# Kernel optimization log

Measured on AMD Instinct MI355X. Metric: run time of the kernel, lower is better.

## Reference

```python
import jax, jax.numpy as jnp
import numpy as np

jax.config.update("jax_enable_x64", True)  # window_sum runs cumsums in double, as in the torch source

WIN = 7
EPS = 0.01


def _gradient(I):
    # forward finite differences, cropping to [D-1, H-1, W-1] (same=False path, reduction='mean')
    c = I[:, :, 1:, 1:, 1:]
    dx = c - I[:, :, :-1, 1:, 1:]
    dy = c - I[:, :, 1:, :-1, 1:]
    dz = c - I[:, :, 1:, 1:, :-1]
    return dx, dy, dz


def _window_sum(I, win):
    # 3D box-filter via triple cumsum on a zero-padded double-precision volume
    if win == 1:
        return I
    half = win // 2
    pad = (half + win % 2, half)
    Ip = jnp.pad(I, ((0, 0), (0, 0), pad, pad, pad)).astype(jnp.float64)
    cs = jnp.cumsum(jnp.cumsum(jnp.cumsum(Ip, axis=2), axis=3), axis=4)
    x, y, z = I.shape[2:]
    w = win
    out = (cs[:, :, w:, w:, w:] - cs[:, :, w:, w:, :z] - cs[:, :, w:, :y, w:]
           - cs[:, :, :x, w:, w:] + cs[:, :, w:, :y, :z] + cs[:, :, :x, w:, :z]
           + cs[:, :, :x, :y, w:] - cs[:, :, :x, :y, :z])
    return out.astype(jnp.float32)


def setup_inputs() -> dict:
    key = jax.random.key(0)
    k1, k2 = jax.random.split(key)
    shape = (2, 1, 160, 192, 160)
    Ii = jax.random.normal(k1, shape, dtype=jnp.float32)
    Ji = jax.random.normal(k2, shape, dtype=jnp.float32)
    return {"Ii": Ii, "Ji": Ji}


def reference(Ii, Ji):
    def det(dx, dy, dz):
        return dx * dx + dy * dy + dz * dz + EPS

    dxI, dyI, dzI = _gradient(Ii)
    dxJ, dyJ, dzJ = _gradient(Ji)
    dx_I = _window_sum(dxI, WIN)
    dy_I = _window_sum(dyI, WIN)
    dz_I = _window_sum(dzI, WIN)
    dx_J = _window_sum(dxJ, WIN)
    dy_J = _window_sum(dyJ, WIN)
    dz_J = _window_sum(dzJ, WIN)
    cross = jnp.abs(dx_I * dx_J + dy_I * dy_J + dz_I * dz_J) + EPS
    norm = jnp.sqrt(det(dx_I, dy_I, dz_I) * det(dx_J, dy_J, dz_J))
    return jnp.mean(cross / norm)
```

## Files before the change

kernel.cpp:

```cpp
#include <hip/hip_runtime.h>

#define IYD 192
#define IZD 160
#define PLANE 30720
#define VOLSZ 4915200
#define YG 191
#define ZG 159

#define RAW_V 660
#define RAW_R 44
#define ZB 1320
#define DB 2400
#define ZD_V 540
#define ZD_R 36
#define TB 3480
#define WB 3992
#define LDSF 4504

#define NVOX_INV (1.0f / 9657342.0f)

__global__ __launch_bounds__(256, 4) void grad_sim_tele(
    const float* __restrict__ Ii, const float* __restrict__ Ji,
    float* __restrict__ out)
{
    __shared__ __align__(16) float lds[LDSF];
    const int tid = threadIdx.x;
    const int z0 = (int)blockIdx.x * 32;
    const int y0 = (int)blockIdx.y * 8;
    const int seg = blockIdx.z & 7;
    const int bat = blockIdx.z >> 3;
    const int s0 = seg * 20;
    const int a0 = (seg == 0) ? 0 : (s0 - 3);
    const int aLast = (seg == 7) ? 159 : (s0 + 23);

    const float* __restrict__ bI = Ii + (size_t)bat * VOLSZ;
    const float* __restrict__ bJ = Ji + (size_t)bat * VOLSZ;

    const float* gp[5];
    int lof[5];
    bool okl[5];
#pragma unroll
    for (int k = 0; k < 5; ++k) {
        int idx = tid + 256 * k;
        bool inr = idx < 1170;
        int id2 = inr ? idx : 0;
        int v = id2 / 585;
        int r = id2 - v * 585;
        int yy = r / 39;
        int zz = r - yy * 39;
        int iy = y0 - 3 + yy;
        int iz = z0 - 3 + zz;
        okl[k] = inr && ((unsigned)iy < IYD) && ((unsigned)iz < IZD);
        int iyc = min(max(iy, 0), IYD - 1);
        int izc = min(max(iz, 0), IZD - 1);
        gp[k] = (v ? bJ : bI) + (iyc * IZD + izc);
        lof[k] = inr ? (v * RAW_V + yy * RAW_R + zz) : 43;
    }

    const int zv = tid / 60;
    const int zrr = tid - 60 * zv;
    const int zr = zrr >> 2;
    const int zq = zrr & 3;
    const bool doZ = tid < 120;
    const bool zlo = (z0 == 0) && (zq == 0);
    const bool zhi = (z0 == 128) && (zq == 3);
    const int rawRd = zv * RAW_V + zr * RAW_R + 8 * zq;
    const int zdWr = zv * ZD_V + zr * ZD_R + 8 * zq;

    const bool doY = tid < 128;
    const int yf = tid >> 5;
    const int yv = yf & 1;
    const int yisW = yf >> 1;
    const int ybase = (yisW ? DB : ZB) + yv * ZD_V + (tid & 31);
    const int yout = (yisW ? WB : TB) + yv * 256 + (tid & 31);

    const int oy = tid >> 5;
    const int oz = tid & 31;
    const int ygl = y0 + oy;
    const int vmax = min(3, 190 - ygl);
    const int vmin = max(-3, -ygl);
    const int relHi = oy + vmax + 4;
    const int relLo = oy + vmin + 3;
    const int vHiI = ZB + relHi * ZD_R + oz;
    const int vLoI = ZB + relLo * ZD_R + oz;
    const bool okyz = (ygl < YG) && ((z0 + oz) < ZG);

    float Tr[2][8], Vr[2][8], Wr[2][8], Sdy[2], Sdz[2];
#pragma unroll
    for (int v = 0; v < 2; ++v) {
#pragma unroll
        for (int j = 0; j < 8; ++j) { Tr[v][j] = 0.f; Vr[v][j] = 0.f; Wr[v][j] = 0.f; }
        Sdy[v] = 0.f; Sdz[v] = 0.f;
    }
    float acc = 0.f;

    {
        const int pb = a0 * PLANE;
        float t[5];
#pragma unroll
        for (int k = 0; k < 5; ++k) t[k] = gp[k][pb];
#pragma unroll
        for (int k = 0; k < 5; ++k) lds[lof[k]] = okl[k] ? t[k] : 0.f;
    }
    __syncthreads();

    for (int ag = (a0 & ~7); ag <= aLast; ag += 8) {
#pragma unroll
        for (int p = 0; p < 8; ++p) {
            const int a = ag + p;
            if (a < a0 || a > aLast) continue;

            const bool dof = (a + 1) <= aLast;
            float pf[5];
            if (dof) {
                const int pb = (a + 1) * PLANE;
#pragma unroll
                for (int k = 0; k < 5; ++k) pf[k] = gp[k][pb];
            }
            if (doZ) {
                float C[16];
                const float4* rb = (const float4*)&lds[rawRd];
#pragma unroll
                for (int u = 0; u < 4; ++u) ((float4*)C)[u] = rb[u];
                float D[8];
#pragma unroll
                for (int i = 0; i < 8; ++i) D[i] = C[i + 7] - C[i];
                if (zlo) { D[0] = C[7] - C[3]; D[1] = C[8] - C[3]; D[2] = C[9] - C[3]; }
                if (zhi) { D[4] = C[10] - C[4]; D[5] = C[10] - C[5];
                           D[6] = C[10] - C[6]; D[7] = C[10] - C[7]; }
                if (zlo) { C[1] = 0.f; C[2] = 0.f; C[3] = 0.f; }
                if (zhi) { C[11] = 0.f; C[12] = 0.f; C[13] = 0.f; C[14] = 0.f; }
                float Z[8];
                float w = C[1] + C[2] + C[3] + C[4] + C[5] + C[6] + C[7];
                Z[0] = w;
#pragma unroll
                for (int m = 1; m < 8; ++m) { w += C[m + 7] - C[m]; Z[m] = w; }
                float4* zb = (float4*)&lds[ZB + zdWr];
                zb[0] = make_float4(Z[0], Z[1], Z[2], Z[3]);
                zb[1] = make_float4(Z[4], Z[5], Z[6], Z[7]);
                float4* db = (float4*)&lds[DB + zdWr];
                db[0] = make_float4(D[0], D[1], D[2], D[3]);
                db[1] = make_float4(D[4], D[5], D[6], D[7]);
            }
            __syncthreads();

            if (doY) {
                float h[15];
#pragma unroll
                for (int r = 1; r < 15; ++r) h[r] = lds[ybase + r * ZD_R];
                if (y0 == 0)   { h[1] = 0.f; h[2] = 0.f; h[3] = 0.f; }
                if (y0 == 184) { h[11] = 0.f; h[12] = 0.f; h[13] = 0.f; h[14] = 0.f; }
                float w = h[1] + h[2] + h[3] + h[4] + h[5] + h[6] + h[7];
                lds[yout] = w;
#pragma unroll
                for (int q = 1; q < 8; ++q) {
                    w += h[q + 7] - h[q];
                    lds[yout + q * 32] = w;
                }
            }
            __syncthreads();

            {
                float tI = lds[TB + tid];
                float tJ = lds[TB + 256 + tid];
                float wI = lds[WB + tid];
                float wJ = lds[WB + 256 + tid];
                float vI = lds[vHiI] - lds[vLoI];
                float vJ = lds[vHiI + ZD_V] - lds[vLoI + ZD_V];
                if (a == a0) { vI = 0.f; vJ = 0.f; wI = 0.f; wJ = 0.f; }
                const int p1 = (p + 1) & 7;
                float hdxI = tI - Tr[0][p1];
                float hdxJ = tJ - Tr[1][p1];
                Sdy[0] += vI - Vr[0][p1]; Vr[0][p] = vI;
                Sdy[1] += vJ - Vr[1][p1]; Vr[1][p] = vJ;
                Sdz[0] += wI - Wr[0][p1]; Wr[0][p] = wI;
                Sdz[1] += wJ - Wr[1][p1]; Wr[1][p] = wJ;
                Tr[0][p] = tI; Tr[1][p] = tJ;
                if (p == 0) {
                    if (a == 0) {
                        Tr[0][5] = tI; Tr[0][6] = tI; Tr[0][7] = tI;
                        Tr[1][5] = tJ; Tr[1][6] = tJ; Tr[1][7] = tJ;
                    }
                }
                if (a >= s0 + 4) {
                    float cross = fabsf(hdxI * hdxJ + Sdy[0] * Sdy[1] + Sdz[0] * Sdz[1]) + 0.01f;
                    float dI = hdxI * hdxI + Sdy[0] * Sdy[0] + Sdz[0] * Sdz[0] + 0.01f;
                    float dJ = hdxJ * hdxJ + Sdy[1] * Sdy[1] + Sdz[1] * Sdz[1] + 0.01f;
                    float val = cross * rsqrtf(dI * dJ);
                    if (okyz) acc += val;
                }
            }
            if (dof) {
#pragma unroll
                for (int k = 0; k < 5; ++k) lds[lof[k]] = okl[k] ? pf[k] : 0.f;
            }
            __syncthreads();
        }
    }

    if (seg == 7) {
#pragma unroll
        for (int t = 0; t < 3; ++t) {
            const int sl = t + 1;
            float hdxI = Tr[0][7] - Tr[0][sl];
            float hdxJ = Tr[1][7] - Tr[1][sl];
            Sdy[0] -= Vr[0][sl]; Sdy[1] -= Vr[1][sl];
            Sdz[0] -= Wr[0][sl]; Sdz[1] -= Wr[1][sl];
            float cross = fabsf(hdxI * hdxJ + Sdy[0] * Sdy[1] + Sdz[0] * Sdz[1]) + 0.01f;
            float dI = hdxI * hdxI + Sdy[0] * Sdy[0] + Sdz[0] * Sdz[0] + 0.01f;
            float dJ = hdxJ * hdxJ + Sdy[1] * Sdy[1] + Sdz[1] * Sdz[1] + 0.01f;
            float val = cross * rsqrtf(dI * dJ);
            if (okyz) acc += val;
        }
    }

#pragma unroll
    for (int off = 32; off > 0; off >>= 1) acc += __shfl_down(acc, off, 64);
    __syncthreads();
    if ((tid & 63) == 0) lds[tid >> 6] = acc;
    __syncthreads();
    if (tid == 0)
        atomicAdd(out, (lds[0] + lds[1] + lds[2] + lds[3]) * NVOX_INV);
}

extern "C" void kernel_launch(void* const* d_in, const int* in_sizes, int n_in,
                              void* d_out, int out_size, void* d_ws, size_t ws_size,
                              hipStream_t stream) {
    const float* Ii = (const float*)d_in[0];
    const float* Ji = (const float*)d_in[1];
    float* out = (float*)d_out;
    hipMemsetAsync(d_out, 0, sizeof(float) * (out_size > 0 ? out_size : 1), stream);
    dim3 grid(5, 24, 16);
    grad_sim_tele<<<grid, dim3(256), 0, stream>>>(Ii, Ji, out);
}
```

Baseline: 86.21 us.

## Restructure box-filter pipeline with 64-wide z tiles and direct float4 global loads

```diff
diff --git a/kernel.cpp b/kernel.cpp
--- a/kernel.cpp
+++ b/kernel.cpp
@@ -7,82 +7,118 @@
 #define YG 191
 #define ZG 159
 
-#define RAW_V 660
-#define RAW_R 44
-#define ZB 1320
-#define DB 2400
-#define ZD_V 540
-#define ZD_R 36
-#define TB 3480
-#define WB 3992
-#define LDSF 4504
+#define ZBV 1020
+#define ZBR 68
+#define YBB 2040
+#define YBV 608
+#define YBR 76
+#define TBB 3256
+#define TBV 544
+#define TBR 68
+#define LDSF 4344
 
 #define NVOX_INV (1.0f / 9657342.0f)
 
-__global__ __launch_bounds__(256, 4) void grad_sim_tele(
+__device__ __forceinline__ float4 f4add(float4 a, float4 b) {
+    return make_float4(a.x + b.x, a.y + b.y, a.z + b.z, a.w + b.w);
+}
+__device__ __forceinline__ float4 f4sub(float4 a, float4 b) {
+    return make_float4(a.x - b.x, a.y - b.y, a.z - b.z, a.w - b.w);
+}
+__device__ __forceinline__ float4 f4scale(float4 a, float s) {
+    return make_float4(a.x * s, a.y * s, a.z * s, a.w * s);
+}
+
+__global__ __launch_bounds__(512, 4) void grad_sim_v9(
     const float* __restrict__ Ii, const float* __restrict__ Ji,
     float* __restrict__ out)
 {
     __shared__ __align__(16) float lds[LDSF];
     const int tid = threadIdx.x;
-    const int z0 = (int)blockIdx.x * 32;
-    const int y0 = (int)blockIdx.y * 8;
-    const int seg = blockIdx.z & 7;
-    const int bat = blockIdx.z >> 3;
-    const int s0 = seg * 20;
+    const int y0 = (int)blockIdx.x * 8;
+    const int z0 = (int)blockIdx.y * 64;
+    const int seg = blockIdx.z % 6;
+    const int bat = blockIdx.z / 6;
+    const int s0 = seg * 27;
     const int a0 = (seg == 0) ? 0 : (s0 - 3);
-    const int aLast = (seg == 7) ? 159 : (s0 + 23);
+    const int aLast = (seg == 5) ? 159 : (s0 + 30);
 
     const float* __restrict__ bI = Ii + (size_t)bat * VOLSZ;
     const float* __restrict__ bJ = Ji + (size_t)bat * VOLSZ;
 
-    const float* gp[5];
-    int lof[5];
-    bool okl[5];
-#pragma unroll
-    for (int k = 0; k < 5; ++k) {
-        int idx = tid + 256 * k;
-        bool inr = idx < 1170;
-        int id2 = inr ? idx : 0;
-        int v = id2 / 585;
-        int r = id2 - v * 585;
-        int yy = r / 39;
-        int zz = r - yy * 39;
-        int iy = y0 - 3 + yy;
-        int iz = z0 - 3 + zz;
-        okl[k] = inr && ((unsigned)iy < IYD) && ((unsigned)iz < IZD);
-        int iyc = min(max(iy, 0), IYD - 1);
-        int izc = min(max(iz, 0), IZD - 1);
-        gp[k] = (v ? bJ : bI) + (iyc * IZD + izc);
-        lof[k] = inr ? (v * RAW_V + yy * RAW_R + zz) : 43;
-    }
-
-    const int zv = tid / 60;
-    const int zrr = tid - 60 * zv;
-    const int zr = zrr >> 2;
-    const int zq = zrr & 3;
-    const bool doZ = tid < 120;
-    const bool zlo = (z0 == 0) && (zq == 0);
-    const bool zhi = (z0 == 128) && (zq == 3);
-    const int rawRd = zv * RAW_V + zr * RAW_R + 8 * zq;
-    const int zdWr = zv * ZD_V + zr * ZD_R + 8 * zq;
-
-    const bool doY = tid < 128;
-    const int yf = tid >> 5;
-    const int yv = yf & 1;
-    const int yisW = yf >> 1;
-    const int ybase = (yisW ? DB : ZB) + yv * ZD_V + (tid & 31);
-    const int yout = (yisW ? WB : TB) + yv * 256 + (tid & 31);
-
-    const int oy = tid >> 5;
-    const int oz = tid & 31;
+    const bool doZB = tid < 240;
+    {
+    }
+    const int e1t = doZB ? tid : 0;
+    const int e1v = e1t / 120;
+    const int e1r = (e1t % 120) >> 3;
+    const int e1o = e1t & 7;
+    const int e1iy = y0 - 3 + e1r;
+    const float e1my = (e1iy >= 0 && e1iy <= 191) ? 1.f : 0.f;
+    const int e1yc = min(max(e1iy, 0), 191);
+    const float* e1p0; const float* e1p1; const float* e1p2; const float* e1p3;
+    float e1m0, e1m1, e1m2, e1m3;
+    {
+        const float* vb = (e1v ? bJ : bI) + e1yc * IZD;
+        int zb;
+        zb = z0 + 8 * e1o - 4;
+        e1m0 = ((zb >= 0) && (zb + 3 <= 159)) ? e1my : 0.f;
+        e1p0 = vb + min(max(zb, 0), 156);
+        zb += 4;
+        e1m1 = ((zb >= 0) && (zb + 3 <= 159)) ? e1my : 0.f;
+        e1p1 = vb + min(max(zb, 0), 156);
+        zb += 4;
+        e1m2 = ((zb >= 0) && (zb + 3 <= 159)) ? e1my : 0.f;
+        e1p2 = vb + min(max(zb, 0), 156);
+        zb += 4;
+        e1m3 = ((zb >= 0) && (zb + 3 <= 159)) ? e1my : 0.f;
+        e1p3 = vb + min(max(zb, 0), 156);
+    }
+    const bool e1zlo = (z0 == 0) && (e1o == 0);
+    const int e1wr = e1v * ZBV + e1r * ZBR + 8 * e1o;
+
+    const int t2 = tid - 384;
+    const bool doYB = (t2 >= 0) && (t2 < 72);
+    const int t2s = doYB ? t2 : 0;
+    const int yv = t2s / 36;
+    const int r36 = t2s % 36;
+    const int yq = r36 >> 1;
+    const int yh = r36 & 1;
+    int yoff[10]; float ymk[10];
+    const float* ybase;
+    {
+        const int yzb = z0 - 4 + 4 * yq;
+        const bool yokq = (yzb >= 0) && (yzb + 3 <= 159);
+        ybase = (yv ? bJ : bI) + min(max(yzb, 0), 156);
+#pragma unroll
+        for (int i = 0; i < 10; ++i) {
+            int iy = y0 + (yh ? 2 : -2) + i;
+            ymk[i] = (yokq && iy >= 1 && iy <= 191) ? 1.f : 0.f;
+            yoff[i] = min(max(iy, 0), 191) * IZD;
+        }
+    }
+    const int ywr = YBB + yv * YBV + (yh * 4) * YBR + 4 * yq;
+
+    const bool doTB = tid < 128;
+    const int bv = tid >> 6;
+    const int br = (tid >> 3) & 7;
+    const int bo = tid & 7;
+    const bool tbzlo = (z0 == 0) && (bo == 0);
+    const int tbRd = YBB + bv * YBV + br * YBR + 8 * bo;
+    const int tbWr = TBB + bv * TBV + br * TBR + 8 * bo;
+
+    const int oy = tid >> 6;
+    const int oz = tid & 63;
     const int ygl = y0 + oy;
     const int vmax = min(3, 190 - ygl);
     const int vmin = max(-3, -ygl);
-    const int relHi = oy + vmax + 4;
-    const int relLo = oy + vmin + 3;
-    const int vHiI = ZB + relHi * ZD_R + oz;
-    const int vLoI = ZB + relLo * ZD_R + oz;
+    const int oVhi = (oy + vmax + 4) * ZBR + oz;
+    const int oVlo = (oy + vmin + 3) * ZBR + oz;
+    const int oT = TBB + oy * TBR + oz;
+    const int relHi = (z0 == 128) ? min(oz + 8, 35) : (oz + 8);
+    const int relLo = max(oz + 1, (z0 == 0) ? 4 : 0);
+    const int oWhi = YBB + oy * YBR + relHi;
+    const int oWlo = YBB + oy * YBR + relLo;
     const bool okyz = (ygl < YG) && ((z0 + oz) < ZG);
 
     float Tr[2][8], Vr[2][8], Wr[2][8], Sdy[2], Sdz[2];
@@ -94,81 +130,89 @@
     }
     float acc = 0.f;
 
-    {
-        const int pb = a0 * PLANE;
-        float t[5];
-#pragma unroll
-        for (int k = 0; k < 5; ++k) t[k] = gp[k][pb];
-#pragma unroll
-        for (int k = 0; k < 5; ++k) lds[lof[k]] = okl[k] ? t[k] : 0.f;
-    }
-    __syncthreads();
+    float4 P0 = make_float4(0, 0, 0, 0), P1 = P0, P2 = P0, P3 = P0;
+    if (doZB) {
+        const size_t pb = (size_t)a0 * PLANE;
+        P0 = *(const float4*)(e1p0 + pb);
+        P1 = *(const float4*)(e1p1 + pb);
+        P2 = *(const float4*)(e1p2 + pb);
+        P3 = *(const float4*)(e1p3 + pb);
+    }
 
     for (int ag = (a0 & ~7); ag <= aLast; ag += 8) {
 #pragma unroll
-        for (int p = 0; p < 8; ++p) {
-            const int a = ag + p;
+        for (int u = 0; u < 8; ++u) {
+            const int a = ag + u;
             if (a < a0 || a > aLast) continue;
 
-            const bool dof = (a + 1) <= aLast;
-            float pf[5];
-            if (dof) {
-                const int pb = (a + 1) * PLANE;
-#pragma unroll
-                for (int k = 0; k < 5; ++k) pf[k] = gp[k][pb];
-            }
-            if (doZ) {
+            if (doZB) {
                 float C[16];
-                const float4* rb = (const float4*)&lds[rawRd];
-#pragma unroll
-                for (int u = 0; u < 4; ++u) ((float4*)C)[u] = rb[u];
-                float D[8];
-#pragma unroll
-                for (int i = 0; i < 8; ++i) D[i] = C[i + 7] - C[i];
-                if (zlo) { D[0] = C[7] - C[3]; D[1] = C[8] - C[3]; D[2] = C[9] - C[3]; }
-                if (zhi) { D[4] = C[10] - C[4]; D[5] = C[10] - C[5];
-                           D[6] = C[10] - C[6]; D[7] = C[10] - C[7]; }
-                if (zlo) { C[1] = 0.f; C[2] = 0.f; C[3] = 0.f; }
-                if (zhi) { C[11] = 0.f; C[12] = 0.f; C[13] = 0.f; C[14] = 0.f; }
+                ((float4*)C)[0] = f4scale(P0, e1m0);
+                ((float4*)C)[1] = f4scale(P1, e1m1);
+                ((float4*)C)[2] = f4scale(P2, e1m2);
+                ((float4*)C)[3] = f4scale(P3, e1m3);
+                if (a + 1 <= aLast) {
+                    const size_t pb = (size_t)(a + 1) * PLANE;
+                    P0 = *(const float4*)(e1p0 + pb);
+                    P1 = *(const float4*)(e1p1 + pb);
+                    P2 = *(const float4*)(e1p2 + pb);
+                    P3 = *(const float4*)(e1p3 + pb);
+                }
+                if (e1zlo) C[4] = 0.f;
                 float Z[8];
-                float w = C[1] + C[2] + C[3] + C[4] + C[5] + C[6] + C[7];
+                float w = C[2] + C[3] + C[4] + C[5] + C[6] + C[7] + C[8];
                 Z[0] = w;
 #pragma unroll
-                for (int m = 1; m < 8; ++m) { w += C[m + 7] - C[m]; Z[m] = w; }
-                float4* zb = (float4*)&lds[ZB + zdWr];
+                for (int m = 1; m < 8; ++m) { w += C[m + 8] - C[m + 1]; Z[m] = w; }
+                float4* zb = (float4*)&lds[e1wr];
                 zb[0] = make_float4(Z[0], Z[1], Z[2], Z[3]);
                 zb[1] = make_float4(Z[4], Z[5], Z[6], Z[7]);
-                float4* db = (float4*)&lds[DB + zdWr];
-                db[0] = make_float4(D[0], D[1], D[2], D[3]);
-                db[1] = make_float4(D[4], D[5], D[6], D[7]);
+            }
+
+            if (doYB) {
+                const size_t pb = (size_t)a * PLANE;
+                float4 R[10];
+#pragma unroll
+                for (int i = 0; i < 10; ++i)
+                    R[i] = f4scale(*(const float4*)(ybase + pb + yoff[i]), ymk[i]);
+                float4 w = f4add(f4add(f4add(R[0], R[1]), f4add(R[2], R[3])),
+                                 f4add(f4add(R[4], R[5]), R[6]));
+                *(float4*)&lds[ywr] = w;
+#pragma unroll
+                for (int m = 1; m < 4; ++m) {
+                    w = f4add(w, f4sub(R[m + 6], R[m - 1]));
+                    *(float4*)&lds[ywr + m * YBR] = w;
+                }
             }
             __syncthreads();
 
-            if (doY) {
-                float h[15];
-#pragma unroll
-                for (int r = 1; r < 15; ++r) h[r] = lds[ybase + r * ZD_R];
-                if (y0 == 0)   { h[1] = 0.f; h[2] = 0.f; h[3] = 0.f; }
-                if (y0 == 184) { h[11] = 0.f; h[12] = 0.f; h[13] = 0.f; h[14] = 0.f; }
-                float w = h[1] + h[2] + h[3] + h[4] + h[5] + h[6] + h[7];
-                lds[yout] = w;
-#pragma unroll
-                for (int q = 1; q < 8; ++q) {
-                    w += h[q + 7] - h[q];
-                    lds[yout + q * 32] = w;
-                }
+            if (doTB) {
+                float C[16];
+                const float4* yb = (const float4*)&lds[tbRd];
+#pragma unroll
+                for (int q = 0; q < 4; ++q) ((float4*)C)[q] = yb[q];
+                if (tbzlo) { C[2] = 0.f; C[3] = 0.f; C[4] = 0.f; }
+                float Z[8];
+                float w = C[2] + C[3] + C[4] + C[5] + C[6] + C[7] + C[8];
+                Z[0] = w;
+#pragma unroll
+                for (int m = 1; m < 8; ++m) { w += C[m + 8] - C[m + 1]; Z[m] = w; }
+                float4* tb = (float4*)&lds[tbWr];
+                tb[0] = make_float4(Z[0], Z[1], Z[2], Z[3]);
+                tb[1] = make_float4(Z[4], Z[5], Z[6], Z[7]);
             }
             __syncthreads();
 
             {
-                float tI = lds[TB + tid];
-                float tJ = lds[TB + 256 + tid];
-                float wI = lds[WB + tid];
-                float wJ = lds[WB + 256 + tid];
-                float vI = lds[vHiI] - lds[vLoI];
-                float vJ = lds[vHiI + ZD_V] - lds[vLoI + ZD_V];
+                float tI = lds[oT];
+                float tJ = lds[oT + TBV];
+                float vI = lds[oVhi] - lds[oVlo];
+                float vJ = lds[oVhi + ZBV] - lds[oVlo + ZBV];
+                float wI = lds[oWhi] - lds[oWlo];
+                float wJ = lds[oWhi + YBV] - lds[oWlo + YBV];
                 if (a == a0) { vI = 0.f; vJ = 0.f; wI = 0.f; wJ = 0.f; }
-                const int p1 = (p + 1) & 7;
+                const int p = u;
+                const int p1 = (u + 1) & 7;
                 float hdxI = tI - Tr[0][p1];
                 float hdxJ = tJ - Tr[1][p1];
                 Sdy[0] += vI - Vr[0][p1]; Vr[0][p] = vI;
@@ -176,11 +220,9 @@
                 Sdz[0] += wI - Wr[0][p1]; Wr[0][p] = wI;
                 Sdz[1] += wJ - Wr[1][p1]; Wr[1][p] = wJ;
                 Tr[0][p] = tI; Tr[1][p] = tJ;
-                if (p == 0) {
-                    if (a == 0) {
-                        Tr[0][5] = tI; Tr[0][6] = tI; Tr[0][7] = tI;
-                        Tr[1][5] = tJ; Tr[1][6] = tJ; Tr[1][7] = tJ;
-                    }
+                if (p == 0 && a == 0) {
+                    Tr[0][5] = tI; Tr[0][6] = tI; Tr[0][7] = tI;
+                    Tr[1][5] = tJ; Tr[1][6] = tJ; Tr[1][7] = tJ;
                 }
                 if (a >= s0 + 4) {
                     float cross = fabsf(hdxI * hdxJ + Sdy[0] * Sdy[1] + Sdz[0] * Sdz[1]) + 0.01f;
@@ -190,18 +232,14 @@
                     if (okyz) acc += val;
                 }
             }
-            if (dof) {
-#pragma unroll
-                for (int k = 0; k < 5; ++k) lds[lof[k]] = okl[k] ? pf[k] : 0.f;
-            }
             __syncthreads();
         }
     }
 
-    if (seg == 7) {
-#pragma unroll
-        for (int t = 0; t < 3; ++t) {
-            const int sl = t + 1;
+    if (seg == 5) {
+#pragma unroll
+        for (int tt = 0; tt < 3; ++tt) {
+            const int sl = tt + 1;
             float hdxI = Tr[0][7] - Tr[0][sl];
             float hdxJ = Tr[1][7] - Tr[1][sl];
             Sdy[0] -= Vr[0][sl]; Sdy[1] -= Vr[1][sl];
@@ -219,8 +257,12 @@
     __syncthreads();
     if ((tid & 63) == 0) lds[tid >> 6] = acc;
     __syncthreads();
-    if (tid == 0)
-        atomicAdd(out, (lds[0] + lds[1] + lds[2] + lds[3]) * NVOX_INV);
+    if (tid == 0) {
+        float total = 0.f;
+#pragma unroll
+        for (int wv = 0; wv < 8; ++wv) total += lds[wv];
+        atomicAdd(out, total * NVOX_INV);
+    }
 }
 
 extern "C" void kernel_launch(void* const* d_in, const int* in_sizes, int n_in,
@@ -230,6 +272,6 @@
     const float* Ji = (const float*)d_in[1];
     float* out = (float*)d_out;
     hipMemsetAsync(d_out, 0, sizeof(float) * (out_size > 0 ? out_size : 1), stream);
-    dim3 grid(5, 24, 16);
-    grad_sim_tele<<<grid, dim3(256), 0, stream>>>(Ii, Ji, out);
-}
+    dim3 grid(24, 3, 12);
+    grad_sim_v9<<<grid, dim3(512), 0, stream>>>(Ii, Ji, out);
+}
```

Result: slower. 249.7 us (+189.6%).
